# Kernel tuning notes

Hardware: AMD Instinct MI355X
Metric: run time of the kernel (lower is better)

Reference implementation:

```python
import jax, jax.numpy as jnp
import numpy as np
import math

N = 32768
C = 128
K = 16
CHUNK = 2048
LN_EPS = float(C)  # original code calls torch.nn.LayerNorm(C, C): second positional arg is eps -> eps = 128.0 (faithful)


def knn_idx(coords):
    """Brute-force KNN on full coords [N,4] (matches knn_points(x_C, x_C, K=16)), chunked over queries."""
    def one_chunk(q):  # q: [CHUNK,4]
        d = jnp.sum((q[:, None, :] - coords[None, :, :]) ** 2, axis=-1)  # [CHUNK,N]
        return jax.lax.top_k(-d, K)[1]  # ascending distance (return_sorted=True)
    qs = coords.reshape(-1, CHUNK, coords.shape[-1])
    return jax.lax.map(one_chunk, qs).reshape(-1, K)  # [N,K]


def layer_norm(x, g, b):
    mu = jnp.mean(x, axis=-1, keepdims=True)
    var = jnp.mean((x - mu) ** 2, axis=-1, keepdims=True)
    return (x - mu) / jnp.sqrt(var + LN_EPS) * g + b


def self_attention(x_f, xyz_enc, new_feature, qw, qb, kw, kb, vw, vb):
    Q = x_f @ qw + qb                              # [N,C]
    nf = new_feature + xyz_enc                     # [N,K,C]
    Kt = nf @ kw + kb                              # [N,K,C]
    scores = jnp.einsum('nkd,nd->nk', Kt, Q) / math.sqrt(C)
    a = jax.nn.softmax(scores, axis=-1)            # [N,K]
    V = nf @ vw + vb                               # [N,K,C]
    return jnp.einsum('nk,nkd->nd', a, V)          # [N,C]


def setup_inputs() -> dict:
    key = jax.random.key(0)
    ks = jax.random.split(key, 22)
    xyz = jax.random.uniform(ks[0], (N, 3), dtype=jnp.float32) * 100.0
    coords = jnp.concatenate([jnp.zeros((N, 1), jnp.float32), xyz], axis=1)  # [N,4] batch col = 0
    feats = jax.random.normal(ks[1], (N, C), dtype=jnp.float32)
    s = 0.02
    def lin(k, din, dout):
        kw, kb = jax.random.split(k)
        return jax.random.normal(kw, (din, dout), jnp.float32) * s, jax.random.normal(kb, (dout,), jnp.float32) * s
    pos_w, pos_b = lin(ks[2], 3, C)
    pos1_w, pos1_b = lin(ks[3], 3, C)
    qw0, qb0 = lin(ks[4], C, C); kw0, kb0 = lin(ks[5], C, C); vw0, vb0 = lin(ks[6], C, C)
    qw1, qb1 = lin(ks[7], C, C); kw1, kb1 = lin(ks[8], C, C); vw1, vb1 = lin(ks[9], C, C)
    lin_w, lin_b = lin(ks[10], C, C)  # MinkowskiConvolution kernel_size=1 == pointwise linear
    return {
        'coords': coords, 'feats': feats,
        'pos_w': pos_w, 'pos_b': pos_b, 'pos1_w': pos1_w, 'pos1_b': pos1_b,
        'qw0': qw0, 'qb0': qb0, 'kw0': kw0, 'kb0': kb0, 'vw0': vw0, 'vb0': vb0,
        'qw1': qw1, 'qb1': qb1, 'kw1': kw1, 'kb1': kb1, 'vw1': vw1, 'vb1': vb1,
        'lin_w': lin_w, 'lin_b': lin_b,
        'g0': jnp.ones((C,), jnp.float32), 'be0': jnp.zeros((C,), jnp.float32),
        'g1': jnp.ones((C,), jnp.float32), 'be1': jnp.zeros((C,), jnp.float32),
    }


def reference(coords, feats, pos_w, pos_b, pos1_w, pos1_b,
              qw0, qb0, kw0, kb0, vw0, vb0,
              qw1, qb1, kw1, kb1, vw1, vb1,
              lin_w, lin_b, g0, be0, g1, be1):
    idx = knn_idx(coords)                           # [N,K]
    xyz = coords[:, 1:]                             # [N,3]
    new_xyz = xyz[:, None, :] - xyz[idx]            # [N,K,3] relative offsets
    # block 1
    xyz_enc = new_xyz @ pos_w + pos_b               # [N,K,C]
    nf = feats[idx]                                 # gather [N,K,C]
    o = self_attention(feats, xyz_enc, nf, qw0, qb0, kw0, kb0, vw0, vb0)
    # block 2: re-gather updated features with same idx
    nf1 = o[idx]
    xyz_enc1 = new_xyz @ pos1_w + pos1_b
    o = self_attention(o, xyz_enc1, nf1, qw1, qb1, kw1, kb1, vw1, vb1)
    # residual + LN, pointwise conv, residual + LN
    h = layer_norm(feats + o, g0, be0)
    h1 = h @ lin_w + lin_b
    return layer_norm(h + h1, g1, be1)
```

## Files before the change

kernel.cpp:

```cpp
#include <hip/hip_runtime.h>
#include <stdint.h>

#define NPT 32768

typedef unsigned int u32;
typedef unsigned short u16;
typedef unsigned long long u64;

typedef short v8s __attribute__((ext_vector_type(8)));
typedef float v4f __attribute__((ext_vector_type(4)));

__device__ __forceinline__ float b2f(u16 u) {
  union { u32 u; float f; } x; x.u = ((u32)u) << 16; return x.f;
}
__device__ __forceinline__ u16 f2b(float f) {
  union { float f; u32 u; } x; x.f = f;
  u32 u = x.u;
  return (u16)((u + 0x7fffu + ((u >> 16) & 1u)) >> 16);
}
__device__ __forceinline__ bool probe_f32(const void* coords) {
  return ((const u16*)coords)[1] == 0;
}
__device__ __forceinline__ float ldany(const void* p, long i, bool f32) {
  return f32 ? ((const float*)p)[i] : b2f(((const u16*)p)[i]);
}
__device__ __forceinline__ float wsum(float v) {
#pragma unroll
  for (int m = 1; m < 64; m <<= 1) v += __shfl_xor(v, m, 64);
  return v;
}
__device__ __forceinline__ v8s ldA8(const void* feats, long row, int off, bool f32) {
  union { uint4 u; v8s s; } c;
  if (f32) {
    const float* f = (const float*)feats + row * 128 + off;
    float4 x = *(const float4*)f;
    float4 y = *(const float4*)(f + 4);
    c.u.x = (u32)f2b(x.x) | ((u32)f2b(x.y) << 16);
    c.u.y = (u32)f2b(x.z) | ((u32)f2b(x.w) << 16);
    c.u.z = (u32)f2b(y.x) | ((u32)f2b(y.y) << 16);
    c.u.w = (u32)f2b(y.z) | ((u32)f2b(y.w) << 16);
  } else {
    c.u = *(const uint4*)((const u16*)feats + row * 128 + off);
  }
  return c.s;
}

#define GC 16
#define GH 6.25f
#define GINV 0.16f
#define NCELL (GC * GC * GC)

__device__ __forceinline__ int cell1d(float v) {
  int c = (int)(v * GINV);
  return c > (GC - 1) ? (GC - 1) : (c < 0 ? 0 : c);
}

__global__ __launch_bounds__(256) void grid_scan(int* __restrict__ cellStart, int* __restrict__ cellPtr) {
  __shared__ int part[256];
  const int t = threadIdx.x;
  int local[16]; int s = 0;
#pragma unroll
  for (int i = 0; i < 16; i++) { local[i] = cellStart[1 + t * 16 + i]; s += local[i]; }
  part[t] = s;
  __syncthreads();
  for (int off = 1; off < 256; off <<= 1) {
    int v = (t >= off) ? part[t - off] : 0;
    __syncthreads();
    part[t] += v;
    __syncthreads();
  }
  int run = (t == 0) ? 0 : part[t - 1];
#pragma unroll
  for (int i = 0; i < 16; i++) {
    int c = t * 16 + i;
    cellPtr[c] = run;
    run += local[i];
    cellStart[c + 1] = run;
  }
}

__global__ __launch_bounds__(256) void grid_scatter(const float* __restrict__ cx, const float* __restrict__ cy,
                                                    const float* __restrict__ cz, const int* __restrict__ pcell,
                                                    int* __restrict__ cellPtr, float4* __restrict__ sortedP,
                                                    int* __restrict__ rank) {
  int i = blockIdx.x * 256 + threadIdx.x;
  int c = pcell[i];
  int pos = atomicAdd(&cellPtr[c], 1);
  sortedP[pos] = make_float4(cx[i], cy[i], cz[i], __int_as_float(i));
  rank[i] = pos;
}

__device__ __forceinline__ void knn_body(int blk, int tid,
                                         const float4* __restrict__ sortedP,
                                         const int* __restrict__ cellStart,
                                         const int* __restrict__ rank,
                                         u16* __restrict__ idxout) {
  const int lane = tid & 63;
  const int gl = lane & 15;
  const int grp = lane >> 4;
  const int q = blk * 16 + (tid >> 4);
  const float4 p = sortedP[q];
  const float qx = p.x, qy = p.y, qz = p.z;
  const int qcx = cell1d(qx), qcy = cell1d(qy), qcz = cell1d(qz);
  const float fx = qx - qcx * GH, fy = qy - qcy * GH, fz = qz - qcz * GH;

  u64 R = ~0ull;

  auto key_of = [&](int g) -> u64 {
    float4 sp = sortedP[g];
    float dx = __fsub_rn(qx, sp.x), dy = __fsub_rn(qy, sp.y), dzc = __fsub_rn(qz, sp.z);
    float d = __fadd_rn(__fadd_rn(__fmul_rn(dx, dx), __fmul_rn(dy, dy)), __fmul_rn(dzc, dzc));
    return ((u64)__float_as_uint(d) << 32) | (u32)__float_as_int(sp.w);
  };

  auto shfl64 = [&](u64 v, int s) -> u64 {
    int lo = __shfl((int)(u32)v, s, 16);
    int hi = __shfl((int)(u32)(v >> 32), s, 16);
    return ((u64)(u32)hi << 32) | (u32)lo;
  };
  auto sxg = [&](u64 v, int m) -> u64 {
    int lo = __shfl_xor((int)(u32)v, m, 64);
    int hi = __shfl_xor((int)(u32)(v >> 32), m, 64);
    return ((u64)(u32)hi << 32) | (u32)lo;
  };
  auto upg = [&](u64 v) -> u64 {
    int lo = __shfl_up((int)(u32)v, 1, 16);
    int hi = __shfl_up((int)(u32)(v >> 32), 1, 16);
    return ((u64)(u32)hi << 32) | (u32)lo;
  };

  auto insert_one = [&](u64 kk) {
    u64 prev = upg(R);
    if (gl == 0) prev = 0ull;
    R = (kk < R) ? ((kk >= prev) ? kk : prev) : R;
  };

  auto batch_merge = [&](u64 key) {
    u64 k15 = shfl64(R, 15);
    u64 mask = __ballot(key < k15);
    u32 mymask = (u32)((mask >> (grp * 16)) & 0xffffu);
    if (mymask == 0) return;
    int pcount = __popc(mymask);
    if (pcount <= 8) {
      u32 mm = mymask;
      while (mm) {
        int s = __ffs((int)mm) - 1;
        mm &= mm - 1;
        insert_one(shfl64(key, s));
      }
      return;
    }
#pragma unroll
    for (int k = 2; k <= 16; k <<= 1) {
#pragma unroll
      for (int j = k >> 1; j > 0; j >>= 1) {
        u64 o = sxg(key, j);
        bool up = ((gl & k) == 0);
        bool lower = ((gl & j) == 0);
        u64 mn = key < o ? key : o;
        u64 mx = key < o ? o : key;
        key = (lower == up) ? mn : mx;
      }
    }
    u64 s = sxg(key, 15);
    u64 mn = R < s ? R : s;
#pragma unroll
    for (int j = 8; j > 0; j >>= 1) {
      u64 o = sxg(mn, j);
      bool lower = ((gl & j) == 0);
      u64 lo = mn < o ? mn : o;
      u64 hi = mn < o ? o : mn;
      mn = lower ? lo : hi;
    }
    R = mn;
  };

  auto scan_range_grp = [&](int s0, int s1) {
    if (s0 >= s1) return;
    int g0 = s0 + gl;
    u64 key = (g0 < s1) ? key_of(g0) : ~0ull;
    for (int base = s0; base < s1; base += 16) {
      int gn = base + 16 + gl;
      u64 nkey = (base + 16 < s1) ? ((gn < s1) ? key_of(gn) : ~0ull) : ~0ull;
      batch_merge(key);
      key = nkey;
    }
  };

  {
    const int xlo = qcx - 1 < 0 ? 0 : qcx - 1;
    const int xhi = qcx + 1 > GC - 1 ? GC - 1 : qcx + 1;
    {
      int rb = (qcz * GC + qcy) * GC;
      scan_range_grp(cellStart[rb + xlo], cellStart[rb + xhi + 1]);
    }
    const int rdz[8] = { 0, 0, -1, 1, -1, -1, 1, 1 };
    const int rdy[8] = { -1, 1, 0, 0, -1, 1, -1, 1 };
#pragma unroll
    for (int s_ = 0; s_ < 8; s_++) {
      int dz = rdz[s_], dy = rdy[s_];
      int z = qcz + dz, y = qcy + dy;
      if (z < 0 || z > GC - 1 || y < 0 || y > GC - 1) continue;
      float gz = (dz == 0) ? 0.f : (dz < 0 ? fz : GH - fz);
      float gy = (dy == 0) ? 0.f : (dy < 0 ? fy : GH - fy);
      float rowb = gz * gz + gy * gy;
      u64 k15 = shfl64(R, 15);
      float d15 = __uint_as_float((u32)(k15 >> 32));
      if (d15 < rowb * 0.998f - 1e-4f) continue;
      int rb = (z * GC + y) * GC;
      scan_range_grp(cellStart[rb + xlo], cellStart[rb + xhi + 1]);
    }
  }

  auto ubound = [&](int rr) -> float {
    float b = 1e30f;
    if (qcx - rr - 1 >= 0) b = fminf(b, fx + rr * GH);
    if (qcx + rr + 1 <= GC - 1) b = fminf(b, (rr + 1) * GH - fx);
    if (qcy - rr - 1 >= 0) b = fminf(b, fy + rr * GH);
    if (qcy + rr + 1 <= GC - 1) b = fminf(b, (rr + 1) * GH - fy);
    if (qcz - rr - 1 >= 0) b = fminf(b, fz + rr * GH);
    if (qcz + rr + 1 <= GC - 1) b = fminf(b, (rr + 1) * GH - fz);
    return b;
  };

  {
    u64 k15 = shfl64(R, 15);
    float d15 = __uint_as_float((u32)(k15 >> 32));
    float b1 = ubound(1);
    bool done = (b1 > 1e29f) || (d15 < b1 * b1 * 0.998f - 1e-4f);
    if (!done) {
      for (int r = 2; r < GC; ++r) {
        int zlo = qcz - r < 0 ? 0 : qcz - r, zhi = qcz + r > GC - 1 ? GC - 1 : qcz + r;
        for (int z = zlo; z <= zhi; ++z) {
          int adz = z - qcz; adz = adz < 0 ? -adz : adz;
          bool ez = (adz == r);
          int ylo = qcy - r < 0 ? 0 : qcy - r, yhi = qcy + r > GC - 1 ? GC - 1 : qcy + r;
          for (int y = ylo; y <= yhi; ++y) {
            int ady = y - qcy; ady = ady < 0 ? -ady : ady;
            bool ey = (ady == r);
            int rb = (z * GC + y) * GC;
            if (ez || ey) {
              int xlo = qcx - r < 0 ? 0 : qcx - r, xhi = qcx + r > GC - 1 ? GC - 1 : qcx + r;
              scan_range_grp(cellStart[rb + xlo], cellStart[rb + xhi + 1]);
            } else {
              int xm = qcx - r, xp = qcx + r;
              if (xm >= 0) scan_range_grp(cellStart[rb + xm], cellStart[rb + xm + 1]);
              if (xp <= GC - 1) scan_range_grp(cellStart[rb + xp], cellStart[rb + xp + 1]);
            }
          }
        }
        k15 = shfl64(R, 15);
        d15 = __uint_as_float((u32)(k15 >> 32));
        float b = ubound(r);
        if (b > 1e29f || d15 < b * b * 0.998f - 1e-4f) break;
      }
    }
  }

  idxout[(size_t)q * 16 + gl] = (u16)rank[(int)(u32)R];
}

__device__ __forceinline__ void gemm_body(int blk, int tid, const void* coords,
                                          const u16* __restrict__ A, const void* __restrict__ featsAny,
                                          const float4* __restrict__ sortedPtr,
                                          const u16* __restrict__ Bf, const void* __restrict__ bias,
                                          u16* __restrict__ Qb, u16* __restrict__ KVb,
                                          const float* __restrict__ tblp, float* __restrict__ pOut,
                                          int ntiles) {
  const bool f32 = probe_f32(coords);
  const int lane = tid & 63;
  const int wave = tid >> 6;
  const int r0 = blk * 64 + wave * 16;
  const int quad = lane >> 4, lr = lane & 15;
  v8s a[4];
  if (sortedPtr) {
    long arow = (long)__float_as_int(sortedPtr[r0 + lr].w);
#pragma unroll
    for (int kq = 0; kq < 4; kq++) a[kq] = ldA8(featsAny, arow, kq * 32 + quad * 8, f32);
  } else {
#pragma unroll
    for (int kq = 0; kq < 4; kq++) {
      union { uint4 u; v8s s; } c;
      c.u = *(const uint4*)(A + (size_t)(r0 + lr) * 128 + kq * 32 + quad * 8);
      a[kq] = c.s;
    }
  }
  float pd0[4] = { 0.f, 0.f, 0.f, 0.f };
  float pd1[4] = { 0.f, 0.f, 0.f, 0.f };
  float pd2[4] = { 0.f, 0.f, 0.f, 0.f };
  float pd3[4] = { 0.f, 0.f, 0.f, 0.f };
  for (int tile = 0; tile < ntiles; ++tile) {
    v4f acc = { 0.f, 0.f, 0.f, 0.f };
#pragma unroll
    for (int kq = 0; kq < 4; kq++) {
      union { uint4 u; v8s s; } c;
      c.u = *(const uint4*)(Bf + ((size_t)(tile * 4 + kq) * 64 + lane) * 8);
      acc = __builtin_amdgcn_mfma_f32_16x16x32_bf16(a[kq], c.s, acc, 0, 0, 0);
    }
    int col = tile * 16 + lr;
    if (col < 128) {
      float bb = ldany(bias, col, f32);
      float t0 = tblp[col], t1 = tblp[128 + col], t2 = tblp[256 + col], t3 = tblp[768 + col];
#pragma unroll
      for (int r = 0; r < 4; r++) {
        float qv = acc[r] + bb;
        Qb[(size_t)(r0 + quad * 4 + r) * 128 + col] = f2b(qv);
        pd0[r] += t0 * qv;
        pd1[r] += t1 * qv;
        pd2[r] += t2 * qv;
        pd3[r] += t3 * qv;
      }
    } else {
#pragma unroll
      for (int r = 0; r < 4; r++) KVb[(size_t)(r0 + quad * 4 + r) * 256 + (col - 128)] = f2b(acc[r]);
    }
  }
  {
#pragma unroll
    for (int m = 1; m < 16; m <<= 1) {
#pragma unroll
      for (int r = 0; r < 4; r++) {
        pd0[r] += __shfl_xor(pd0[r], m, 64);
        pd1[r] += __shfl_xor(pd1[r], m, 64);
        pd2[r] += __shfl_xor(pd2[r], m, 64);
        pd3[r] += __shfl_xor(pd3[r], m, 64);
      }
    }
    if (lr < 4) {
#pragma unroll
      for (int r = 0; r < 4; r++) {
        float v = (lr == 0) ? pd0[r] : ((lr == 1) ? pd1[r] : ((lr == 2) ? pd2[r] : pd3[r]));
        pOut[(size_t)(r0 + quad * 4 + r) * 4 + lr] = v;
      }
    }
  }
}

__global__ __launch_bounds__(256) void knn_gemm0(const float4* __restrict__ sortedP,
                                                 const int* __restrict__ cellStart,
                                                 const int* __restrict__ rank,
                                                 u16* __restrict__ idxout,
                                                 const void* __restrict__ coords,
                                                 const void* __restrict__ feats,
                                                 const u16* __restrict__ Bf, const void* __restrict__ bias,
                                                 u16* __restrict__ Qb, u16* __restrict__ KVb,
                                                 const float* __restrict__ tblp, float* __restrict__ pOut) {
  if (blockIdx.x < 2048) {
    knn_body(blockIdx.x, threadIdx.x, sortedP, cellStart, rank, idxout);
  } else {
    gemm_body(blockIdx.x - 2048, threadIdx.x, coords, (const u16*)nullptr, feats, sortedP,
              Bf, bias, Qb, KVb, tblp, pOut, 24);
  }
}

__global__ __launch_bounds__(256) void gemm_kernel(const void* __restrict__ coords,
                                                   const u16* __restrict__ A, const u16* __restrict__ Bf,
                                                   const void* __restrict__ bias, u16* __restrict__ Qb,
                                                   u16* __restrict__ KVb,
                                                   const float* __restrict__ tblp, float* __restrict__ pOut,
                                                   int ntiles) {
  gemm_body(blockIdx.x, threadIdx.x, coords, A, (const void*)nullptr, (const float4*)nullptr,
            Bf, bias, Qb, KVb, tblp, pOut, ntiles);
}

__global__ __launch_bounds__(256) void gemm_ln(const void* __restrict__ coords,
                                               const u16* __restrict__ A ,
                                               const u16* __restrict__ Bf, const void* __restrict__ bias,
                                               const float4* __restrict__ sortedP,
                                               const void* __restrict__ g, const void* __restrict__ be,
                                               void* __restrict__ outAny) {
  const bool f32 = probe_f32(coords);
  const int lane = threadIdx.x & 63;
  const int wave = threadIdx.x >> 6;
  const int r0 = blockIdx.x * 64 + wave * 16;
  const int quad = lane >> 4, lr = lane & 15;
  v8s a[4];
#pragma unroll
  for (int kq = 0; kq < 4; kq++) {
    union { uint4 u; v8s s; } c;
    c.u = *(const uint4*)(A + (size_t)(r0 + lr) * 128 + kq * 32 + quad * 8);
    a[kq] = c.s;
  }
  float xv[8][4];
#pragma unroll
  for (int tile = 0; tile < 8; ++tile) {
    v4f acc = { 0.f, 0.f, 0.f, 0.f };
#pragma unroll
    for (int kq = 0; kq < 4; kq++) {
      union { uint4 u; v8s s; } c;
      c.u = *(const uint4*)(Bf + ((size_t)(tile * 4 + kq) * 64 + lane) * 8);
      acc = __builtin_amdgcn_mfma_f32_16x16x32_bf16(a[kq], c.s, acc, 0, 0, 0);
    }
    int col = tile * 16 + lr;
    float bb = ldany(bias, col, f32);
#pragma unroll
    for (int r = 0; r < 4; r++) {
      float h = b2f(A[(size_t)(r0 + quad * 4 + r) * 128 + col]);
      xv[tile][r] = h + acc[r] + bb;
    }
  }
  float sum[4];
#pragma unroll
  for (int r = 0; r < 4; r++) {
    sum[r] = 0.f;
#pragma unroll
    for (int tile = 0; tile < 8; ++tile) sum[r] += xv[tile][r];
  }
#pragma unroll
  for (int m = 1; m < 16; m <<= 1) {
#pragma unroll
    for (int r = 0; r < 4; r++) sum[r] += __shfl_xor(sum[r], m, 64);
  }
  float mu[4];
#pragma unroll
  for (int r = 0; r < 4; r++) mu[r] = sum[r] * (1.f / 128.f);
  float vs[4];
#pragma unroll
  for (int r = 0; r < 4; r++) {
    vs[r] = 0.f;
#pragma unroll
    for (int tile = 0; tile < 8; ++tile) {
      float d = xv[tile][r] - mu[r];
      vs[r] += d * d;
    }
  }
#pragma unroll
  for (int m = 1; m < 16; m <<= 1) {
#pragma unroll
    for (int r = 0; r < 4; r++) vs[r] += __shfl_xor(vs[r], m, 64);
  }
  float rinv[4];
#pragma unroll
  for (int r = 0; r < 4; r++) rinv[r] = 1.0f / sqrtf(vs[r] * (1.f / 128.f) + 128.0f);
  long orig[4];
#pragma unroll
  for (int r = 0; r < 4; r++) orig[r] = (long)__float_as_int(sortedP[r0 + quad * 4 + r].w);
#pragma unroll
  for (int tile = 0; tile < 8; ++tile) {
    int col = tile * 16 + lr;
    float gv = ldany(g, col, f32), bv = ldany(be, col, f32);
#pragma unroll
    for (int r = 0; r < 4; r++) {
      float y = (xv[tile][r] - mu[r]) * rinv[r] * gv + bv;
      if (f32) ((float*)outAny)[orig[r] * 128 + col] = y;
      else ((u16*)outAny)[orig[r] * 128 + col] = f2b(y);
    }
  }
}

__global__ __launch_bounds__(256) void prep_all(
    const void* coords,
    const void* pw0, const void* pb0, const void* kw0, const void* kb0, const void* vw0, const void* vb0,
    const void* pw1, const void* pb1, const void* kw1, const void* kb1, const void* vw1, const void* vb1,
    float* __restrict__ tbl, int* __restrict__ cellStart,
    float* __restrict__ cx, float* __restrict__ cy, float* __restrict__ cz, int* __restrict__ pcell,
    const void* __restrict__ qw0, const void* __restrict__ qw1, const void* __restrict__ linw,
    u16* __restrict__ Bf0, u16* __restrict__ Bf1, u16* __restrict__ BfL) {
  const bool f32 = probe_f32(coords);
  if (blockIdx.x < 512) {
    const int lane = threadIdx.x & 63;
    const int o = blockIdx.x * 4 + (threadIdx.x >> 6);
    const int l = o >> 10;
    const int rem = o & 1023;
    const void* PW = l ? pw1 : pw0;
    const void* PB = l ? pb1 : pb0;
    const void* KW = l ? kw1 : kw0;
    const void* KB = l ? kb1 : kb0;
    const void* VW = l ? vw1 : vw0;
    const void* VB = l ? vb1 : vb0;
    float acc, extra = 0.f;
    if (rem < 768) {
      bool isV = rem >= 384;
      int r2 = isV ? rem - 384 : rem;
      int i = r2 >> 7, c = r2 & 127;
      const void* W = isV ? VW : KW;
      acc = ldany(PW, i * 128 + lane, f32) * ldany(W, (long)lane * 128 + c, f32)
          + ldany(PW, i * 128 + lane + 64, f32) * ldany(W, (long)(lane + 64) * 128 + c, f32);
    } else {
      bool isV = rem >= 896;
      int c = rem & 127;
      const void* W = isV ? VW : KW;
      const void* B = isV ? VB : KB;
      acc = ldany(PB, lane, f32) * ldany(W, (long)lane * 128 + c, f32)
          + ldany(PB, lane + 64, f32) * ldany(W, (long)(lane + 64) * 128 + c, f32);
      extra = ldany(B, c, f32);
    }
    acc = wsum(acc) + extra;
    if (lane == 0) tbl[l * 1024 + rem] = acc;
  } else if (blockIdx.x < 640) {
    int i = (blockIdx.x - 512) * 256 + threadIdx.x;
    float x = ldany(coords, (long)i * 4 + 1, f32);
    float y = ldany(coords, (long)i * 4 + 2, f32);
    float z = ldany(coords, (long)i * 4 + 3, f32);
    cx[i] = x; cy[i] = y; cz[i] = z;
    int c = (cell1d(z) * GC + cell1d(y)) * GC + cell1d(x);
    pcell[i] = c;
    atomicAdd(&cellStart[c + 1], 1);
  } else {
    int tid = (blockIdx.x - 640) * 256 + threadIdx.x;
    const void *w0, *w1, *w2; u16* out; int t;
    if (tid < 49152) { t = tid; w0 = qw0; w1 = kw0; w2 = vw0; out = Bf0; }
    else if (tid < 98304) { t = tid - 49152; w0 = qw1; w1 = kw1; w2 = vw1; out = Bf1; }
    else { t = tid - 98304; w0 = linw; w1 = linw; w2 = linw; out = BfL; }
    int j = t & 7, lane = (t >> 3) & 63, kq = (t >> 9) & 3, tile = t >> 11;
    int k = kq * 32 + ((lane >> 4) << 3) + j;
    int col = tile * 16 + (lane & 15);
    const void* w = (col < 128) ? w0 : ((col < 256) ? w1 : w2);
    long off = (long)k * 128 + (col & 127);
    out[t] = f32 ? f2b(((const float*)w)[off]) : ((const u16*)w)[off];
  }
}

__global__ __launch_bounds__(256) void attn_kernel(const void* __restrict__ coordsRaw,
                                                   const float4* __restrict__ sortedP,
                                                   const u16* __restrict__ idx,
                                                   const u16* __restrict__ Qb, const u16* __restrict__ KVb,
                                                   const float* __restrict__ tbl, const float* __restrict__ p4,
                                                   const void* __restrict__ feats,
                                                   const void* __restrict__ g, const void* __restrict__ be,
                                                   u16* __restrict__ outB, int mode) {
  const int lane = threadIdx.x & 63;
  const int swz = (blockIdx.x & 7) * (gridDim.x >> 3) + (blockIdx.x >> 3);
  const int n = swz * 4 + (threadIdx.x >> 6);
  const int c0 = 2 * lane;
  const int k = lane & 15;
  const int quad = lane >> 4;
  const int base = lane & 48;

  const int j = idx[(size_t)n * 16 + k];
  u32 vr[16];
#pragma unroll
  for (int k2 = 0; k2 < 16; k2++) {
    int jk = __shfl(j, base + k2, 64);
    vr[k2] = *(const u32*)(KVb + (size_t)jk * 256 + 128 + c0);
  }
  uint4 kf[4];
#pragma unroll
  for (int kq = 0; kq < 4; kq++) {
    kf[kq] = *(const uint4*)(KVb + (size_t)j * 256 + kq * 32 + quad * 8);
  }
  const float4 P = sortedP[n];
  const float4 Pj = sortedP[j];
  const float nx = P.x - Pj.x, ny = P.y - Pj.y, nz = P.z - Pj.z;
  const float4 pv = *(const float4*)(p4 + (size_t)n * 4);

  v4f sacc = { 0.f, 0.f, 0.f, 0.f };
#pragma unroll
  for (int kq = 0; kq < 4; kq++) {
    union { uint4 u; v8s s; } ka, qa;
    ka.u = kf[kq];
    qa.u = *(const uint4*)(Qb + (size_t)n * 128 + kq * 32 + quad * 8);
    sacc = __builtin_amdgcn_mfma_f32_16x16x32_bf16(ka.s, qa.s, sacc, 0, 0, 0);
  }
  const int srcl = ((k >> 2) << 4) | k;
  float t0 = __shfl(sacc[0], srcl, 64);
  float t1 = __shfl(sacc[1], srcl, 64);
  float t2 = __shfl(sacc[2], srcl, 64);
  float t3 = __shfl(sacc[3], srcl, 64);
  float s = (k & 2) ? ((k & 1) ? t3 : t2) : ((k & 1) ? t1 : t0);
  float sc = (s + nx * pv.x + ny * pv.y + nz * pv.z + pv.w) * 0.08838834764831845f;

  float mx = sc;
#pragma unroll
  for (int m = 1; m < 16; m <<= 1) mx = fmaxf(mx, __shfl_xor(mx, m, 64));
  float e = expf(sc - mx);
  float ssum = e;
#pragma unroll
  for (int m = 1; m < 16; m <<= 1) ssum += __shfl_xor(ssum, m, 64);
  const float a = e / ssum;

  float wx = a * nx, wy = a * ny, wz = a * nz;
#pragma unroll
  for (int m = 1; m < 16; m <<= 1) {
    wx += __shfl_xor(wx, m, 64);
    wy += __shfl_xor(wy, m, 64);
    wz += __shfl_xor(wz, m, 64);
  }

  float a0 = 0.f, a1 = 0.f;
#pragma unroll
  for (int k2 = 0; k2 < 16; k2++) {
    float ak = __shfl(a, base + k2, 64);
    u32 u = vr[k2];
    a0 += ak * b2f((u16)(u & 0xffffu));
    a1 += ak * b2f((u16)(u >> 16));
  }
  float o0 = a0 + wx * tbl[384 + c0] + wy * tbl[512 + c0] + wz * tbl[640 + c0] + tbl[896 + c0];
  float o1 = a1 + wx * tbl[384 + c0 + 1] + wy * tbl[512 + c0 + 1] + wz * tbl[640 + c0 + 1] + tbl[896 + c0 + 1];
  if (mode == 1) {
    const bool f32 = probe_f32(coordsRaw);
    long orig = (long)__float_as_int(P.w);
    float x0 = ldany(feats, orig * 128 + c0, f32) + o0;
    float x1 = ldany(feats, orig * 128 + c0 + 1, f32) + o1;
    float mu = wsum(x0 + x1) * (1.f / 128.f);
    float d0 = x0 - mu, d1 = x1 - mu;
    float var = wsum(d0 * d0 + d1 * d1) * (1.f / 128.f);
    float rinv = 1.0f / sqrtf(var + 128.0f);
    o0 = d0 * rinv * ldany(g, c0, f32) + ldany(be, c0, f32);
    o1 = d1 * rinv * ldany(g, c0 + 1, f32) + ldany(be, c0 + 1, f32);
  }
  ((u32*)outB)[(size_t)n * 64 + lane] = (u32)f2b(o0) | ((u32)f2b(o1) << 16);
}

extern "C" void kernel_launch(void* const* d_in, const int* in_sizes, int n_in,
                              void* d_out, int out_size, void* d_ws, size_t ws_size,
                              hipStream_t stream) {
  (void)in_sizes; (void)n_in; (void)out_size; (void)ws_size;
  const void* coords = d_in[0];
  const void* feats = d_in[1];
  const void* pos_w = d_in[2];
  const void* pos_b = d_in[3];
  const void* pos1_w = d_in[4];
  const void* pos1_b = d_in[5];
  const void* qw0 = d_in[6];
  const void* qb0 = d_in[7];
  const void* kw0 = d_in[8];
  const void* kb0 = d_in[9];
  const void* vw0 = d_in[10];
  const void* vb0 = d_in[11];
  const void* qw1 = d_in[12];
  const void* qb1 = d_in[13];
  const void* kw1 = d_in[14];
  const void* kb1 = d_in[15];
  const void* vw1 = d_in[16];
  const void* vb1 = d_in[17];
  const void* lin_w = d_in[18];
  const void* lin_b = d_in[19];
  const void* g0 = d_in[20];
  const void* be0 = d_in[21];
  const void* g1 = d_in[22];
  const void* be1 = d_in[23];

  char* w = (char*)d_ws;
  u16* idxp = (u16*)(w + 0);
  float4* sortedP = (float4*)(w + 1048576);
  int* rank = (int*)(w + 1572864);
  float* cx = (float*)(w + 1703936);
  float* cy = (float*)(w + 1835008);
  float* cz = (float*)(w + 1966080);
  float* tbl = (float*)(w + 2097152);
  u16* Bf0 = (u16*)(w + 2105344);
  u16* Bf1 = (u16*)(w + 2203648);
  u16* BfL = (u16*)(w + 2301952);
  float* p4 = (float*)(w + 2334720);
  int* cellStart = (int*)(w + 2859008);
  int* cellPtr = (int*)(w + 2875456);
  int* pcell = (int*)(w + 2891840);
  u16* oS = (u16*)(w + 10723328);
  u16* Qb = (u16*)(w + 19111936);
  u16* KVb = (u16*)(w + 27500544);

  hipMemsetAsync(cellStart, 0, (NCELL + 1) * sizeof(int), stream);

  hipLaunchKernelGGL(prep_all, dim3(1088), dim3(256), 0, stream, coords,
                     pos_w, pos_b, kw0, kb0, vw0, vb0, pos1_w, pos1_b, kw1, kb1, vw1, vb1,
                     tbl, cellStart, cx, cy, cz, pcell, qw0, qw1, lin_w, Bf0, Bf1, BfL);

  hipLaunchKernelGGL(grid_scan, dim3(1), dim3(256), 0, stream, cellStart, cellPtr);
  hipLaunchKernelGGL(grid_scatter, dim3(128), dim3(256), 0, stream, cx, cy, cz, pcell, cellPtr, sortedP, rank);

  hipLaunchKernelGGL(knn_gemm0, dim3(2560), dim3(256), 0, stream, sortedP, cellStart, rank, idxp,
                     coords, feats, Bf0, qb0, Qb, KVb, tbl, p4);

  hipLaunchKernelGGL(attn_kernel, dim3(8192), dim3(256), 0, stream, coords, sortedP, idxp, Qb, KVb, tbl, p4,
                     (const void*)nullptr, (const void*)nullptr, (const void*)nullptr, oS, 0);
  hipLaunchKernelGGL(gemm_kernel, dim3(512), dim3(256), 0, stream, coords, oS, Bf1, qb1, Qb, KVb,
                     tbl + 1024, p4, 24);
  hipLaunchKernelGGL(attn_kernel, dim3(8192), dim3(256), 0, stream, coords, sortedP, idxp, Qb, KVb, tbl + 1024, p4,
                     feats, g0, be0, oS, 1);
  hipLaunchKernelGGL(gemm_ln, dim3(512), dim3(256), 0, stream, coords, oS, BfL, lin_b, sortedP, g1, be1, d_out);
}
```

Baseline: 285.9 us.

## Switch KNN from 16-lane cooperative groups to one thread per query

Replaces the 16-lane-per-query KNN (shuffle-based bitonic batch merge plus a ballot-driven insert path) with one thread per query that keeps a sorted 16-entry register array and does insertion-sort updates. The KNN part of the fused knn/gemm kernel drops from 2048 blocks to 128 blocks. This removes cross-lane shuffle and ballot overhead but serializes each candidate scan within a thread. It also raises register pressure (16 u64 values) and causes divergence between queries that scan different numbers of cells.

```diff
diff --git a/kernel.cpp b/kernel.cpp
--- a/kernel.cpp
+++ b/kernel.cpp
@@ -90,21 +90,19 @@
   rank[i] = pos;
 }
 
-__device__ __forceinline__ void knn_body(int blk, int tid,
+__device__ __forceinline__ void knn_body(int q,
                                          const float4* __restrict__ sortedP,
                                          const int* __restrict__ cellStart,
                                          const int* __restrict__ rank,
                                          u16* __restrict__ idxout) {
-  const int lane = tid & 63;
-  const int gl = lane & 15;
-  const int grp = lane >> 4;
-  const int q = blk * 16 + (tid >> 4);
   const float4 p = sortedP[q];
   const float qx = p.x, qy = p.y, qz = p.z;
   const int qcx = cell1d(qx), qcy = cell1d(qy), qcz = cell1d(qz);
   const float fx = qx - qcx * GH, fy = qy - qcy * GH, fz = qz - qcz * GH;
 
-  u64 R = ~0ull;
+  u64 R[16];
+#pragma unroll
+  for (int i = 0; i < 16; i++) R[i] = ~0ull;
 
   auto key_of = [&](int g) -> u64 {
     float4 sp = sortedP[g];
@@ -113,78 +111,17 @@
     return ((u64)__float_as_uint(d) << 32) | (u32)__float_as_int(sp.w);
   };
 
-  auto shfl64 = [&](u64 v, int s) -> u64 {
-    int lo = __shfl((int)(u32)v, s, 16);
-    int hi = __shfl((int)(u32)(v >> 32), s, 16);
-    return ((u64)(u32)hi << 32) | (u32)lo;
+  auto insert = [&](u64 key) {
+    if (key < R[15]) {
+#pragma unroll
+      for (int i = 15; i >= 1; --i)
+        R[i] = (key >= R[i]) ? R[i] : ((key >= R[i - 1]) ? key : R[i - 1]);
+      R[0] = (key < R[0]) ? key : R[0];
+    }
   };
-  auto sxg = [&](u64 v, int m) -> u64 {
-    int lo = __shfl_xor((int)(u32)v, m, 64);
-    int hi = __shfl_xor((int)(u32)(v >> 32), m, 64);
-    return ((u64)(u32)hi << 32) | (u32)lo;
-  };
-  auto upg = [&](u64 v) -> u64 {
-    int lo = __shfl_up((int)(u32)v, 1, 16);
-    int hi = __shfl_up((int)(u32)(v >> 32), 1, 16);
-    return ((u64)(u32)hi << 32) | (u32)lo;
-  };
-
-  auto insert_one = [&](u64 kk) {
-    u64 prev = upg(R);
-    if (gl == 0) prev = 0ull;
-    R = (kk < R) ? ((kk >= prev) ? kk : prev) : R;
-  };
-
-  auto batch_merge = [&](u64 key) {
-    u64 k15 = shfl64(R, 15);
-    u64 mask = __ballot(key < k15);
-    u32 mymask = (u32)((mask >> (grp * 16)) & 0xffffu);
-    if (mymask == 0) return;
-    int pcount = __popc(mymask);
-    if (pcount <= 8) {
-      u32 mm = mymask;
-      while (mm) {
-        int s = __ffs((int)mm) - 1;
-        mm &= mm - 1;
-        insert_one(shfl64(key, s));
-      }
-      return;
-    }
-#pragma unroll
-    for (int k = 2; k <= 16; k <<= 1) {
-#pragma unroll
-      for (int j = k >> 1; j > 0; j >>= 1) {
-        u64 o = sxg(key, j);
-        bool up = ((gl & k) == 0);
-        bool lower = ((gl & j) == 0);
-        u64 mn = key < o ? key : o;
-        u64 mx = key < o ? o : key;
-        key = (lower == up) ? mn : mx;
-      }
-    }
-    u64 s = sxg(key, 15);
-    u64 mn = R < s ? R : s;
-#pragma unroll
-    for (int j = 8; j > 0; j >>= 1) {
-      u64 o = sxg(mn, j);
-      bool lower = ((gl & j) == 0);
-      u64 lo = mn < o ? mn : o;
-      u64 hi = mn < o ? o : mn;
-      mn = lower ? lo : hi;
-    }
-    R = mn;
-  };
-
-  auto scan_range_grp = [&](int s0, int s1) {
-    if (s0 >= s1) return;
-    int g0 = s0 + gl;
-    u64 key = (g0 < s1) ? key_of(g0) : ~0ull;
-    for (int base = s0; base < s1; base += 16) {
-      int gn = base + 16 + gl;
-      u64 nkey = (base + 16 < s1) ? ((gn < s1) ? key_of(gn) : ~0ull) : ~0ull;
-      batch_merge(key);
-      key = nkey;
-    }
+
+  auto scan_range = [&](int s0, int s1) {
+    for (int g = s0; g < s1; ++g) insert(key_of(g));
   };
 
   {
@@ -192,7 +129,7 @@
     const int xhi = qcx + 1 > GC - 1 ? GC - 1 : qcx + 1;
     {
       int rb = (qcz * GC + qcy) * GC;
-      scan_range_grp(cellStart[rb + xlo], cellStart[rb + xhi + 1]);
+      scan_range(cellStart[rb + xlo], cellStart[rb + xhi + 1]);
     }
     const int rdz[8] = { 0, 0, -1, 1, -1, -1, 1, 1 };
     const int rdy[8] = { -1, 1, 0, 0, -1, 1, -1, 1 };
@@ -204,11 +141,10 @@
       float gz = (dz == 0) ? 0.f : (dz < 0 ? fz : GH - fz);
       float gy = (dy == 0) ? 0.f : (dy < 0 ? fy : GH - fy);
       float rowb = gz * gz + gy * gy;
-      u64 k15 = shfl64(R, 15);
-      float d15 = __uint_as_float((u32)(k15 >> 32));
+      float d15 = __uint_as_float((u32)(R[15] >> 32));
       if (d15 < rowb * 0.998f - 1e-4f) continue;
       int rb = (z * GC + y) * GC;
-      scan_range_grp(cellStart[rb + xlo], cellStart[rb + xhi + 1]);
+      scan_range(cellStart[rb + xlo], cellStart[rb + xhi + 1]);
     }
   }
 
@@ -224,8 +160,7 @@
   };
 
   {
-    u64 k15 = shfl64(R, 15);
-    float d15 = __uint_as_float((u32)(k15 >> 32));
+    float d15 = __uint_as_float((u32)(R[15] >> 32));
     float b1 = ubound(1);
     bool done = (b1 > 1e29f) || (d15 < b1 * b1 * 0.998f - 1e-4f);
     if (!done) {
@@ -241,23 +176,23 @@
             int rb = (z * GC + y) * GC;
             if (ez || ey) {
               int xlo = qcx - r < 0 ? 0 : qcx - r, xhi = qcx + r > GC - 1 ? GC - 1 : qcx + r;
-              scan_range_grp(cellStart[rb + xlo], cellStart[rb + xhi + 1]);
+              scan_range(cellStart[rb + xlo], cellStart[rb + xhi + 1]);
             } else {
               int xm = qcx - r, xp = qcx + r;
-              if (xm >= 0) scan_range_grp(cellStart[rb + xm], cellStart[rb + xm + 1]);
-              if (xp <= GC - 1) scan_range_grp(cellStart[rb + xp], cellStart[rb + xp + 1]);
+              if (xm >= 0) scan_range(cellStart[rb + xm], cellStart[rb + xm + 1]);
+              if (xp <= GC - 1) scan_range(cellStart[rb + xp], cellStart[rb + xp + 1]);
             }
           }
         }
-        k15 = shfl64(R, 15);
-        d15 = __uint_as_float((u32)(k15 >> 32));
+        d15 = __uint_as_float((u32)(R[15] >> 32));
         float b = ubound(r);
         if (b > 1e29f || d15 < b * b * 0.998f - 1e-4f) break;
       }
     }
   }
 
-  idxout[(size_t)q * 16 + gl] = (u16)rank[(int)(u32)R];
+#pragma unroll
+  for (int i = 0; i < 16; i++) idxout[(size_t)q * 16 + i] = (u16)rank[(int)(u32)R[i]];
 }
 
 __device__ __forceinline__ void gemm_body(int blk, int tid, const void* coords,
@@ -345,10 +280,10 @@
                                                  const u16* __restrict__ Bf, const void* __restrict__ bias,
                                                  u16* __restrict__ Qb, u16* __restrict__ KVb,
                                                  const float* __restrict__ tblp, float* __restrict__ pOut) {
-  if (blockIdx.x < 2048) {
-    knn_body(blockIdx.x, threadIdx.x, sortedP, cellStart, rank, idxout);
+  if (blockIdx.x < 128) {
+    knn_body(blockIdx.x * 256 + threadIdx.x, sortedP, cellStart, rank, idxout);
   } else {
-    gemm_body(blockIdx.x - 2048, threadIdx.x, coords, (const u16*)nullptr, feats, sortedP,
+    gemm_body(blockIdx.x - 128, threadIdx.x, coords, (const u16*)nullptr, feats, sortedP,
               Bf, bias, Qb, KVb, tblp, pOut, 24);
   }
 }
@@ -659,7 +594,7 @@
   hipLaunchKernelGGL(grid_scan, dim3(1), dim3(256), 0, stream, cellStart, cellPtr);
   hipLaunchKernelGGL(grid_scatter, dim3(128), dim3(256), 0, stream, cx, cy, cz, pcell, cellPtr, sortedP, rank);
 
-  hipLaunchKernelGGL(knn_gemm0, dim3(2560), dim3(256), 0, stream, sortedP, cellStart, rank, idxp,
+  hipLaunchKernelGGL(knn_gemm0, dim3(640), dim3(256), 0, stream, sortedP, cellStart, rank, idxp,
                      coords, feats, Bf0, qb0, Qb, KVb, tbl, p4);
 
   hipLaunchKernelGGL(attn_kernel, dim3(8192), dim3(256), 0, stream, coords, sortedP, idxp, Qb, KVb, tbl, p4,
```

After: 398.5 us. 1.39x slower.
